# Kernel optimization log

Hardware: AMD Instinct MI355X
Metric: run time of the kernel (lower is better)

## Reference

```python
import jax, jax.numpy as jnp
import numpy as np

STATE_SIZE = 29
ACTION_SIZE = 3


def setup_inputs() -> dict:
    key = jax.random.key(0)
    ks = jax.random.split(key, 12)

    def row_norm(k, shape, scale=1.0):
        w = jax.random.normal(k, shape, dtype=jnp.float32)
        return w * (scale / jnp.sqrt(jnp.sum(w * w, axis=1, keepdims=True)))

    lrelu_gain = float(np.sqrt(2.0 / (1.0 + 0.01 ** 2)))  # torch calculate_gain('leaky_relu')
    inp = {
        "x": jax.random.normal(ks[0], (1, STATE_SIZE), dtype=jnp.float32),
        "hx": jnp.zeros((1, 128), jnp.float32),
        "cx": jnp.zeros((1, 128), jnp.float32),
        "w1": row_norm(ks[1], (256, STATE_SIZE)) * lrelu_gain,
        "b1": jnp.zeros((256,), jnp.float32),
        "w2": row_norm(ks[2], (256, 256)) * lrelu_gain,
        "b2": jnp.zeros((256,), jnp.float32),
        "w3": row_norm(ks[3], (128, 256)) * lrelu_gain,
        "b3": jnp.zeros((128,), jnp.float32),
        "w4": row_norm(ks[4], (128, 128)) * lrelu_gain,
        "b4": jnp.zeros((128,), jnp.float32),
        "w_ih": jax.random.normal(ks[5], (512, 128), dtype=jnp.float32) * 0.08,
        "b_ih": jnp.zeros((512,), jnp.float32),
        "w_hh": jax.random.normal(ks[6], (512, 128), dtype=jnp.float32) * 0.08,
        "b_hh": jnp.zeros((512,), jnp.float32),
        "w_critic": row_norm(ks[7], (1, 128), 1.0),
        "b_critic": jnp.zeros((1,), jnp.float32),
        "w_actor": row_norm(ks[8], (ACTION_SIZE, 128), 0.01),
        "b_actor": jnp.zeros((ACTION_SIZE,), jnp.float32),
        "w_actor2": row_norm(ks[9], (ACTION_SIZE, 128), 0.01),
        "b_actor2": jnp.zeros((ACTION_SIZE,), jnp.float32),
    }
    return inp


def _lrelu(v):
    return jnp.where(v > 0, v, 0.1 * v)


def reference(x, hx, cx, w1, b1, w2, b2, w3, b3, w4, b4,
              w_ih, b_ih, w_hh, b_hh,
              w_critic, b_critic, w_actor, b_actor, w_actor2, b_actor2):
    h = _lrelu(x @ w1.T + b1)
    h = _lrelu(h @ w2.T + b2)
    h = _lrelu(h @ w3.T + b3)
    h = _lrelu(h @ w4.T + b4)            # [1,128]
    # LSTMCell: gate order i, f, g, o (PyTorch convention)
    gates = h @ w_ih.T + b_ih + hx @ w_hh.T + b_hh  # [1,512]
    i, f, g, o = jnp.split(gates, 4, axis=-1)
    c_new = jax.nn.sigmoid(f) * cx + jax.nn.sigmoid(i) * jnp.tanh(g)
    h_new = jax.nn.sigmoid(o) * jnp.tanh(c_new)      # [1,128]
    value = jnp.squeeze(h_new @ w_critic.T + b_critic)          # scalar
    actor = jax.nn.soft_sign(h_new @ w_actor.T + b_actor)
    actor = jnp.squeeze(actor)                                   # [action_size]
    actor2 = jnp.squeeze(h_new @ w_actor2.T + b_actor2)         # [action_size]
    return (value, actor, actor2)
```

## Files before the change

kernel.cpp:

```cpp
#include <hip/hip_runtime.h>
#include <math.h>


#define NB_G 8
#define NB_M 16
#define NB   (NB_G + NB_M)
#define TPB  256
#define MAGIC 0x3A3C5A17u

__device__ __forceinline__ float lrelu(float v) { return v > 0.f ? v : 0.1f * v; }
__device__ __forceinline__ float sigm(float v)  { return 1.f / (1.f + __expf(-v)); }
__device__ __forceinline__ float dot4(float4 a, float4 b) {
    return a.x * b.x + a.y * b.y + a.z * b.z + a.w * b.w;
}

__device__ __forceinline__ void send(unsigned long long* p, float v) {
    unsigned lo = __float_as_uint(v);
    unsigned long long pk = (unsigned long long)lo |
                            ((unsigned long long)(lo ^ MAGIC) << 32);
    __hip_atomic_store(p, pk, __ATOMIC_RELAXED, __HIP_MEMORY_SCOPE_AGENT);
}
__device__ __forceinline__ float recv(unsigned long long* p) {
    for (;;) {
        unsigned long long pk =
            __hip_atomic_load(p, __ATOMIC_RELAXED, __HIP_MEMORY_SCOPE_AGENT);
        unsigned lo = (unsigned)pk, hi = (unsigned)(pk >> 32);
        if ((lo ^ MAGIC) == hi) return __uint_as_float(lo);
    }
}

__global__ __launch_bounds__(TPB, 1) void a3c_fwd(
    const float* __restrict__ x, const float* __restrict__ hx, const float* __restrict__ cx,
    const float* __restrict__ w1, const float* __restrict__ b1,
    const float* __restrict__ w2, const float* __restrict__ b2,
    const float* __restrict__ w3, const float* __restrict__ b3,
    const float* __restrict__ w4, const float* __restrict__ b4,
    const float* __restrict__ w_ih, const float* __restrict__ b_ih,
    const float* __restrict__ w_hh, const float* __restrict__ b_hh,
    const float* __restrict__ w_critic, const float* __restrict__ b_critic,
    const float* __restrict__ w_actor, const float* __restrict__ b_actor,
    const float* __restrict__ w_actor2, const float* __restrict__ b_actor2,
    float* __restrict__ out, unsigned long long* __restrict__ wsp)
{
    unsigned long long* ws_h2 = wsp;
    unsigned long long* ws_h3 = wsp + 256;
    unsigned long long* ws_gt = wsp + 384;

    const int blk = blockIdx.x, tid = threadIdx.x;

    if (blk >= NB_G) {
        const int gid = (blk - NB_G) * TPB + tid;

        __shared__ __align__(16) float x_s[32];
        __shared__ __align__(16) float h1_s[256];
        __shared__ __align__(16) float h2_s[256];

        float a1[29];
        {
            const float* w1r = w1 + tid * 29;
            #pragma unroll
            for (int j = 0; j < 29; ++j) a1[j] = w1r[j];
        }
        const int r2 = gid >> 4, p2 = gid & 15;
        float4 a2[4];
        {
            const float4* wp = (const float4*)(w2 + r2 * 256 + p2 * 16);
            #pragma unroll
            for (int j = 0; j < 4; ++j) a2[j] = wp[j];
        }
        const int r3 = gid >> 5, p3 = gid & 31;
        float4 a3v[2];
        {
            const float4* wp = (const float4*)(w3 + r3 * 256 + p3 * 8);
            a3v[0] = wp[0]; a3v[1] = wp[1];
        }
        const float bb1 = b1[tid], bb2 = b2[r2], bb3 = b3[r3];

        if (tid < 29) x_s[tid] = x[tid];
        __syncthreads();

        {
            float s = 0.f;
            #pragma unroll
            for (int j = 0; j < 29; ++j) s += a1[j] * x_s[j];
            h1_s[tid] = lrelu(s + bb1);
        }
        __syncthreads();

        {
            const float4* hp = (const float4*)(h1_s + p2 * 16);
            float s = 0.f;
            #pragma unroll
            for (int j = 0; j < 4; ++j) s += dot4(a2[j], hp[j]);
            s += __shfl_xor(s, 1); s += __shfl_xor(s, 2);
            s += __shfl_xor(s, 4); s += __shfl_xor(s, 8);
            if (p2 == 0) send(ws_h2 + r2, lrelu(s + bb2));
        }

        h2_s[tid] = recv(ws_h2 + tid);
        __syncthreads();

        {
            const float4* hp = (const float4*)(h2_s + p3 * 8);
            float s = dot4(a3v[0], hp[0]) + dot4(a3v[1], hp[1]);
            s += __shfl_xor(s, 1); s += __shfl_xor(s, 2);
            s += __shfl_xor(s, 4); s += __shfl_xor(s, 8);
            s += __shfl_xor(s, 16);
            if (p3 == 0) send(ws_h3 + r3, lrelu(s + bb3));
        }
        return;
    }

    const int row = blk * 64 + (tid >> 2), p = tid & 3;
    const int r4  = tid >> 1, p4 = tid & 1;

    __shared__ __align__(16) float hx_s[128];
    __shared__ __align__(16) float h3_s[128];
    __shared__ __align__(16) float h4_s[128];
    __shared__ __align__(16) float gates_s[512];
    __shared__ __align__(16) float hn_s[128];
    __shared__ __align__(16) float head_s[896];
    __shared__ __align__(16) float hb_s[8];

    if (tid < 128) hx_s[tid] = hx[tid];

    float4 ah[8];
    {
        const float4* wp = (const float4*)(w_hh + row * 128 + p * 32);
        #pragma unroll
        for (int j = 0; j < 8; ++j) ah[j] = wp[j];
    }
    float4 a4[16];
    {
        const float4* wp = (const float4*)(w4 + r4 * 128 + p4 * 64);
        #pragma unroll
        for (int j = 0; j < 16; ++j) a4[j] = wp[j];
    }
    float4 ai[8];
    {
        const float4* wp = (const float4*)(w_ih + row * 128 + p * 32);
        #pragma unroll
        for (int j = 0; j < 8; ++j) ai[j] = wp[j];
    }
    const float bsum = b_ih[row] + b_hh[row];
    const float bb4  = b4[r4];

    float cval = 0.f;
    if (blk == 0) {
        if (tid < 32)        ((float4*)head_s)[tid] = ((const float4*)w_critic)[tid];
        else if (tid < 128)  ((float4*)head_s)[tid] = ((const float4*)w_actor)[tid - 32];
        else if (tid < 224)  ((float4*)head_s)[tid] = ((const float4*)w_actor2)[tid - 128];
        else if (tid == 224) hb_s[0] = b_critic[0];
        else if (tid < 228)  hb_s[tid - 224] = b_actor[tid - 225];
        else if (tid < 231)  hb_s[tid - 224] = b_actor2[tid - 228];
        if (tid < 128) cval = cx[tid];
    }
    __syncthreads();

    float g0;
    {
        const float4* hv = (const float4*)(hx_s + p * 32);
        float s = 0.f;
        #pragma unroll
        for (int j = 0; j < 8; ++j) s += dot4(ah[j], hv[j]);
        s += __shfl_xor(s, 1); s += __shfl_xor(s, 2);
        g0 = s + bsum;
    }

    if (tid < 128) h3_s[tid] = recv(ws_h3 + tid);
    __syncthreads();

    {
        const float4* hp = (const float4*)(h3_s + p4 * 64);
        float s = 0.f;
        #pragma unroll
        for (int j = 0; j < 16; ++j) s += dot4(a4[j], hp[j]);
        s += __shfl_xor(s, 1);
        if (p4 == 0) h4_s[r4] = lrelu(s + bb4);
    }
    __syncthreads();

    {
        const float4* hp = (const float4*)(h4_s + p * 32);
        float s = 0.f;
        #pragma unroll
        for (int j = 0; j < 8; ++j) s += dot4(ai[j], hp[j]);
        s += __shfl_xor(s, 1); s += __shfl_xor(s, 2);
        if (p == 0) send(ws_gt + row, g0 + s);
    }

    if (blk == 0) {
        gates_s[tid]       = recv(ws_gt + tid);
        gates_s[tid + 256] = recv(ws_gt + tid + 256);
        __syncthreads();
        if (tid < 128) {
            float ig = gates_s[tid];
            float fg = gates_s[tid + 128];
            float gg = gates_s[tid + 256];
            float og = gates_s[tid + 384];
            float c  = sigm(fg) * cval + sigm(ig) * tanhf(gg);
            hn_s[tid] = sigm(og) * tanhf(c);
        }
        __syncthreads();
        if (tid < 64) {
            #pragma unroll
            for (int o = 0; o < 7; ++o) {
                const float* wrow = head_s + o * 128;
                float s = hn_s[tid] * wrow[tid] + hn_s[tid + 64] * wrow[tid + 64];
                #pragma unroll
                for (int m = 1; m < 64; m <<= 1) s += __shfl_xor(s, m);
                if (tid == 0) {
                    float r = s + hb_s[o];
                    if (o >= 1 && o <= 3) r = r / (1.f + fabsf(r));
                    out[o] = r;
                }
            }
        }
    }
}

extern "C" void kernel_launch(void* const* d_in, const int* in_sizes, int n_in,
                              void* d_out, int out_size, void* d_ws, size_t ws_size,
                              hipStream_t stream) {
    const float* x        = (const float*)d_in[0];
    const float* hx       = (const float*)d_in[1];
    const float* cx       = (const float*)d_in[2];
    const float* w1       = (const float*)d_in[3];
    const float* b1       = (const float*)d_in[4];
    const float* w2       = (const float*)d_in[5];
    const float* b2       = (const float*)d_in[6];
    const float* w3       = (const float*)d_in[7];
    const float* b3       = (const float*)d_in[8];
    const float* w4       = (const float*)d_in[9];
    const float* b4       = (const float*)d_in[10];
    const float* w_ih     = (const float*)d_in[11];
    const float* b_ih     = (const float*)d_in[12];
    const float* w_hh     = (const float*)d_in[13];
    const float* b_hh     = (const float*)d_in[14];
    const float* w_critic = (const float*)d_in[15];
    const float* b_critic = (const float*)d_in[16];
    const float* w_actor  = (const float*)d_in[17];
    const float* b_actor  = (const float*)d_in[18];
    const float* w_actor2 = (const float*)d_in[19];
    const float* b_actor2 = (const float*)d_in[20];
    float* out = (float*)d_out;
    unsigned long long* wsp = (unsigned long long*)d_ws;

    a3c_fwd<<<NB, TPB, 0, stream>>>(x, hx, cx, w1, b1, w2, b2, w3, b3, w4, b4,
                                    w_ih, b_ih, w_hh, b_hh,
                                    w_critic, b_critic, w_actor, b_actor,
                                    w_actor2, b_actor2, out, wsp);
}
```

Before: 102.3 us.

## Split each MLP/LSTM layer across dedicated block groups with cross-block dataflow

Restructures the persistent kernel from 24 blocks (8 gate blocks, 16 MLP blocks with redundant layer-1 compute) into 96 blocks, each group owning one layer: w1, w2, w3, w4 and the LSTM gates. Activations pass between groups through the tagged workspace slots with spin-wait receives. The intent is to spread weight loads over more CUs so each thread holds fewer registers and per-block latency drops. In exchange there are more cross-block handoff stages, an extra global round-trip for h1 and h4, and a dependency on all 96 blocks being co-resident so the spin-waits cannot deadlock.

```diff
diff --git a/kernel.cpp b/kernel.cpp
--- a/kernel.cpp
+++ b/kernel.cpp
@@ -2,11 +2,15 @@
 #include <math.h>
 
 
-#define NB_G 8
-#define NB_M 16
-#define NB   (NB_G + NB_M)
+#define NB   96
 #define TPB  256
 #define MAGIC 0x3A3C5A17u
+
+#define H1_OFF 0
+#define H2_OFF 256
+#define H3_OFF 512
+#define H4_OFF 640
+#define GT_OFF 768
 
 __device__ __forceinline__ float lrelu(float v) { return v > 0.f ? v : 0.1f * v; }
 __device__ __forceinline__ float sigm(float v)  { return 1.f / (1.f + __expf(-v)); }
@@ -42,179 +46,177 @@
     const float* __restrict__ w_actor2, const float* __restrict__ b_actor2,
     float* __restrict__ out, unsigned long long* __restrict__ wsp)
 {
-    unsigned long long* ws_h2 = wsp;
-    unsigned long long* ws_h3 = wsp + 256;
-    unsigned long long* ws_gt = wsp + 384;
-
     const int blk = blockIdx.x, tid = threadIdx.x;
 
-    if (blk >= NB_G) {
-        const int gid = (blk - NB_G) * TPB + tid;
+    if (blk < 8) {
+        const int row = blk * 32 + (tid >> 3), sub = tid & 7;
+        float a[4];
+        #pragma unroll
+        for (int j = 0; j < 4; ++j) {
+            int c = sub * 4 + j;
+            a[j] = (c < 29) ? w1[row * 29 + c] : 0.f;
+        }
+        const float bb1 = b1[row];
 
         __shared__ __align__(16) float x_s[32];
+        __shared__ __align__(16) float head_s[896];
+        __shared__ __align__(16) float hb_s[8];
+        __shared__ __align__(16) float cx_s[128];
+        __shared__ __align__(16) float gates_s[512];
+        __shared__ __align__(16) float hn_s[128];
+
+        if (tid < 32) x_s[tid] = (tid < 29) ? x[tid] : 0.f;
+        if (blk == 0) {
+            if (tid < 32)        ((float4*)head_s)[tid] = ((const float4*)w_critic)[tid];
+            else if (tid < 128)  ((float4*)head_s)[tid] = ((const float4*)w_actor)[tid - 32];
+            else if (tid < 224)  ((float4*)head_s)[tid] = ((const float4*)w_actor2)[tid - 128];
+            else if (tid == 224) hb_s[0] = b_critic[0];
+            else if (tid < 228)  hb_s[tid - 224] = b_actor[tid - 225];
+            else if (tid < 231)  hb_s[tid - 224] = b_actor2[tid - 228];
+            if (tid >= 64 && tid < 192) cx_s[tid - 64] = cx[tid - 64];
+        }
+        __syncthreads();
+
+        {
+            const float* xp = x_s + sub * 4;
+            float s = a[0] * xp[0] + a[1] * xp[1] + a[2] * xp[2] + a[3] * xp[3];
+            s += __shfl_xor(s, 1); s += __shfl_xor(s, 2); s += __shfl_xor(s, 4);
+            if (sub == 0) send(wsp + H1_OFF + row, lrelu(s + bb1));
+        }
+
+        if (blk == 0) {
+            gates_s[tid]       = recv(wsp + GT_OFF + tid);
+            gates_s[tid + 256] = recv(wsp + GT_OFF + tid + 256);
+            __syncthreads();
+            if (tid < 128) {
+                float ig = gates_s[tid];
+                float fg = gates_s[tid + 128];
+                float gg = gates_s[tid + 256];
+                float og = gates_s[tid + 384];
+                float c  = sigm(fg) * cx_s[tid] + sigm(ig) * tanhf(gg);
+                hn_s[tid] = sigm(og) * tanhf(c);
+            }
+            __syncthreads();
+            if (tid < 64) {
+                #pragma unroll
+                for (int o = 0; o < 7; ++o) {
+                    const float* wrow = head_s + o * 128;
+                    float s = hn_s[tid] * wrow[tid] + hn_s[tid + 64] * wrow[tid + 64];
+                    #pragma unroll
+                    for (int m = 1; m < 64; m <<= 1) s += __shfl_xor(s, m);
+                    if (tid == 0) {
+                        float r = s + hb_s[o];
+                        if (o >= 1 && o <= 3) r = r / (1.f + fabsf(r));
+                        out[o] = r;
+                    }
+                }
+            }
+        }
+        return;
+    }
+
+    if (blk < 40) {
+        const int row = (blk - 8) * 8 + (tid >> 5), p = tid & 31;
+        float4 a0, a1v;
+        {
+            const float4* wp = (const float4*)(w2 + row * 256 + p * 8);
+            a0 = wp[0]; a1v = wp[1];
+        }
+        const float bb2 = b2[row];
+
         __shared__ __align__(16) float h1_s[256];
+        h1_s[tid] = recv(wsp + H1_OFF + tid);
+        __syncthreads();
+
+        const float4* hp = (const float4*)(h1_s + p * 8);
+        float s = dot4(a0, hp[0]) + dot4(a1v, hp[1]);
+        s += __shfl_xor(s, 1); s += __shfl_xor(s, 2);
+        s += __shfl_xor(s, 4); s += __shfl_xor(s, 8);
+        s += __shfl_xor(s, 16);
+        if (p == 0) send(wsp + H2_OFF + row, lrelu(s + bb2));
+        return;
+    }
+
+    if (blk < 56) {
+        const int row = (blk - 40) * 8 + (tid >> 5), p = tid & 31;
+        float4 a0, a1v;
+        {
+            const float4* wp = (const float4*)(w3 + row * 256 + p * 8);
+            a0 = wp[0]; a1v = wp[1];
+        }
+        const float bb3 = b3[row];
+
         __shared__ __align__(16) float h2_s[256];
-
-        float a1[29];
-        {
-            const float* w1r = w1 + tid * 29;
-            #pragma unroll
-            for (int j = 0; j < 29; ++j) a1[j] = w1r[j];
-        }
-        const int r2 = gid >> 4, p2 = gid & 15;
-        float4 a2[4];
-        {
-            const float4* wp = (const float4*)(w2 + r2 * 256 + p2 * 16);
-            #pragma unroll
-            for (int j = 0; j < 4; ++j) a2[j] = wp[j];
-        }
-        const int r3 = gid >> 5, p3 = gid & 31;
-        float4 a3v[2];
-        {
-            const float4* wp = (const float4*)(w3 + r3 * 256 + p3 * 8);
-            a3v[0] = wp[0]; a3v[1] = wp[1];
-        }
-        const float bb1 = b1[tid], bb2 = b2[r2], bb3 = b3[r3];
-
-        if (tid < 29) x_s[tid] = x[tid];
-        __syncthreads();
-
-        {
-            float s = 0.f;
-            #pragma unroll
-            for (int j = 0; j < 29; ++j) s += a1[j] * x_s[j];
-            h1_s[tid] = lrelu(s + bb1);
-        }
-        __syncthreads();
-
-        {
-            const float4* hp = (const float4*)(h1_s + p2 * 16);
-            float s = 0.f;
-            #pragma unroll
-            for (int j = 0; j < 4; ++j) s += dot4(a2[j], hp[j]);
+        h2_s[tid] = recv(wsp + H2_OFF + tid);
+        __syncthreads();
+
+        const float4* hp = (const float4*)(h2_s + p * 8);
+        float s = dot4(a0, hp[0]) + dot4(a1v, hp[1]);
+        s += __shfl_xor(s, 1); s += __shfl_xor(s, 2);
+        s += __shfl_xor(s, 4); s += __shfl_xor(s, 8);
+        s += __shfl_xor(s, 16);
+        if (p == 0) send(wsp + H3_OFF + row, lrelu(s + bb3));
+        return;
+    }
+
+    if (blk < 64) {
+        const int row = (blk - 56) * 16 + (tid >> 4), p = tid & 15;
+        float4 a0, a1v;
+        {
+            const float4* wp = (const float4*)(w4 + row * 128 + p * 8);
+            a0 = wp[0]; a1v = wp[1];
+        }
+        const float bb4 = b4[row];
+
+        __shared__ __align__(16) float h3_s[128];
+        if (tid < 128) h3_s[tid] = recv(wsp + H3_OFF + tid);
+        __syncthreads();
+
+        const float4* hp = (const float4*)(h3_s + p * 8);
+        float s = dot4(a0, hp[0]) + dot4(a1v, hp[1]);
+        s += __shfl_xor(s, 1); s += __shfl_xor(s, 2);
+        s += __shfl_xor(s, 4); s += __shfl_xor(s, 8);
+        if (p == 0) send(wsp + H4_OFF + row, lrelu(s + bb4));
+        return;
+    }
+
+    {
+        const int row = (blk - 64) * 16 + (tid >> 4), p = tid & 15;
+        float4 ah0, ah1;
+        {
+            const float4* wp = (const float4*)(w_hh + row * 128 + p * 8);
+            ah0 = wp[0]; ah1 = wp[1];
+        }
+        float4 ai0, ai1;
+        {
+            const float4* wp = (const float4*)(w_ih + row * 128 + p * 8);
+            ai0 = wp[0]; ai1 = wp[1];
+        }
+        const float bsum = b_ih[row] + b_hh[row];
+
+        __shared__ __align__(16) float hx_s[128];
+        __shared__ __align__(16) float h4_s[128];
+        if (tid < 128) hx_s[tid] = hx[tid];
+        __syncthreads();
+
+        float g0;
+        {
+            const float4* hp = (const float4*)(hx_s + p * 8);
+            float s = dot4(ah0, hp[0]) + dot4(ah1, hp[1]);
             s += __shfl_xor(s, 1); s += __shfl_xor(s, 2);
             s += __shfl_xor(s, 4); s += __shfl_xor(s, 8);
-            if (p2 == 0) send(ws_h2 + r2, lrelu(s + bb2));
-        }
-
-        h2_s[tid] = recv(ws_h2 + tid);
-        __syncthreads();
-
-        {
-            const float4* hp = (const float4*)(h2_s + p3 * 8);
-            float s = dot4(a3v[0], hp[0]) + dot4(a3v[1], hp[1]);
+            g0 = s + bsum;
+        }
+
+        if (tid < 128) h4_s[tid] = recv(wsp + H4_OFF + tid);
+        __syncthreads();
+
+        {
+            const float4* hp = (const float4*)(h4_s + p * 8);
+            float s = dot4(ai0, hp[0]) + dot4(ai1, hp[1]);
             s += __shfl_xor(s, 1); s += __shfl_xor(s, 2);
             s += __shfl_xor(s, 4); s += __shfl_xor(s, 8);
-            s += __shfl_xor(s, 16);
-            if (p3 == 0) send(ws_h3 + r3, lrelu(s + bb3));
-        }
-        return;
-    }
-
-    const int row = blk * 64 + (tid >> 2), p = tid & 3;
-    const int r4  = tid >> 1, p4 = tid & 1;
-
-    __shared__ __align__(16) float hx_s[128];
-    __shared__ __align__(16) float h3_s[128];
-    __shared__ __align__(16) float h4_s[128];
-    __shared__ __align__(16) float gates_s[512];
-    __shared__ __align__(16) float hn_s[128];
-    __shared__ __align__(16) float head_s[896];
-    __shared__ __align__(16) float hb_s[8];
-
-    if (tid < 128) hx_s[tid] = hx[tid];
-
-    float4 ah[8];
-    {
-        const float4* wp = (const float4*)(w_hh + row * 128 + p * 32);
-        #pragma unroll
-        for (int j = 0; j < 8; ++j) ah[j] = wp[j];
-    }
-    float4 a4[16];
-    {
-        const float4* wp = (const float4*)(w4 + r4 * 128 + p4 * 64);
-        #pragma unroll
-        for (int j = 0; j < 16; ++j) a4[j] = wp[j];
-    }
-    float4 ai[8];
-    {
-        const float4* wp = (const float4*)(w_ih + row * 128 + p * 32);
-        #pragma unroll
-        for (int j = 0; j < 8; ++j) ai[j] = wp[j];
-    }
-    const float bsum = b_ih[row] + b_hh[row];
-    const float bb4  = b4[r4];
-
-    float cval = 0.f;
-    if (blk == 0) {
-        if (tid < 32)        ((float4*)head_s)[tid] = ((const float4*)w_critic)[tid];
-        else if (tid < 128)  ((float4*)head_s)[tid] = ((const float4*)w_actor)[tid - 32];
-        else if (tid < 224)  ((float4*)head_s)[tid] = ((const float4*)w_actor2)[tid - 128];
-        else if (tid == 224) hb_s[0] = b_critic[0];
-        else if (tid < 228)  hb_s[tid - 224] = b_actor[tid - 225];
-        else if (tid < 231)  hb_s[tid - 224] = b_actor2[tid - 228];
-        if (tid < 128) cval = cx[tid];
-    }
-    __syncthreads();
-
-    float g0;
-    {
-        const float4* hv = (const float4*)(hx_s + p * 32);
-        float s = 0.f;
-        #pragma unroll
-        for (int j = 0; j < 8; ++j) s += dot4(ah[j], hv[j]);
-        s += __shfl_xor(s, 1); s += __shfl_xor(s, 2);
-        g0 = s + bsum;
-    }
-
-    if (tid < 128) h3_s[tid] = recv(ws_h3 + tid);
-    __syncthreads();
-
-    {
-        const float4* hp = (const float4*)(h3_s + p4 * 64);
-        float s = 0.f;
-        #pragma unroll
-        for (int j = 0; j < 16; ++j) s += dot4(a4[j], hp[j]);
-        s += __shfl_xor(s, 1);
-        if (p4 == 0) h4_s[r4] = lrelu(s + bb4);
-    }
-    __syncthreads();
-
-    {
-        const float4* hp = (const float4*)(h4_s + p * 32);
-        float s = 0.f;
-        #pragma unroll
-        for (int j = 0; j < 8; ++j) s += dot4(ai[j], hp[j]);
-        s += __shfl_xor(s, 1); s += __shfl_xor(s, 2);
-        if (p == 0) send(ws_gt + row, g0 + s);
-    }
-
-    if (blk == 0) {
-        gates_s[tid]       = recv(ws_gt + tid);
-        gates_s[tid + 256] = recv(ws_gt + tid + 256);
-        __syncthreads();
-        if (tid < 128) {
-            float ig = gates_s[tid];
-            float fg = gates_s[tid + 128];
-            float gg = gates_s[tid + 256];
-            float og = gates_s[tid + 384];
-            float c  = sigm(fg) * cval + sigm(ig) * tanhf(gg);
-            hn_s[tid] = sigm(og) * tanhf(c);
-        }
-        __syncthreads();
-        if (tid < 64) {
-            #pragma unroll
-            for (int o = 0; o < 7; ++o) {
-                const float* wrow = head_s + o * 128;
-                float s = hn_s[tid] * wrow[tid] + hn_s[tid + 64] * wrow[tid + 64];
-                #pragma unroll
-                for (int m = 1; m < 64; m <<= 1) s += __shfl_xor(s, m);
-                if (tid == 0) {
-                    float r = s + hb_s[o];
-                    if (o >= 1 && o <= 3) r = r / (1.f + fabsf(r));
-                    out[o] = r;
-                }
-            }
+            if (p == 0) send(wsp + GT_OFF + row, g0 + s);
         }
     }
 }
```

Measured after the change: 104.8 us. +2.5%, slower.
